# Optimization experiments

Hardware: AMD Instinct MI355X
Metric: run time of the kernel (lower is better)

## Reference

```python
import jax, jax.numpy as jnp
import numpy as np

B, L1, L2, D = 32, 512, 512, 1024


def setup_inputs() -> dict:
    key = jax.random.key(0)
    k1, k2, k3, k4 = jax.random.split(key, 4)
    v1 = jax.random.normal(k1, (B, L1, D), dtype=jnp.float32)
    v2 = jax.random.normal(k2, (B, L2, D), dtype=jnp.float32)
    # row/column is fully masked (which would NaN the softmax).
    v1_mask = jax.random.uniform(k3, (B, L1)) < 0.2
    v2_mask = jax.random.uniform(k4, (B, L2)) < 0.2
    return {"v1": v1, "v2": v2, "v1_mask": v1_mask, "v2_mask": v2_mask}


def reference(v1, v2, v1_mask, v2_mask):
    # similarity: [B, L1, L2]
    sim = jnp.einsum("bid,bjd->bij", v1, v2)
    neg_inf = jnp.float32(-jnp.inf)
    # softmax over v2 positions (dim=2), masking padded v2 columns
    v1_v2_attn = jax.nn.softmax(
        jnp.where(v2_mask[:, None, :], neg_inf, sim), axis=2)
    # softmax over v1 positions (dim=1), masking padded v1 rows
    v2_v1_attn = jax.nn.softmax(
        jnp.where(v1_mask[:, :, None], neg_inf, sim), axis=1)
    attended_v1 = jnp.einsum("bij,bjd->bid", v1_v2_attn, v2)  # [B,L1,D]
    attended_v2 = jnp.einsum("bij,bid->bjd", v2_v1_attn, v1)  # [B,L2,D]
    attended_v1 = jnp.where(v1_mask[:, :, None], 0.0, attended_v1)
    attended_v2 = jnp.where(v2_mask[:, :, None], 0.0, attended_v2)
    return attended_v1, attended_v2
```

## Files before the change

### kernel.cpp

```cpp
#include <hip/hip_runtime.h>
#include <stdint.h>


#define Bn 32
#define Ln 512
#define Dn 1024

typedef __attribute__((ext_vector_type(4))) float f32x4;
typedef __attribute__((ext_vector_type(4))) unsigned short u16x4;
typedef __attribute__((ext_vector_type(8))) unsigned short u16x8;
typedef __attribute__((ext_vector_type(8))) __bf16 bf16x8;

__device__ __forceinline__ unsigned short f2bf(float f) {
  unsigned int u = __float_as_uint(f);
  u += 0x7FFFu + ((u >> 16) & 1u);
  return (unsigned short)(u >> 16);
}

__device__ __forceinline__ void async_cp16(const void* g, void* l) {
  __builtin_amdgcn_global_load_lds(
      (__attribute__((address_space(1))) void*)(g),
      (__attribute__((address_space(3))) void*)(l), 16, 0, 0);
}

__device__ __forceinline__ void split8(f32x4 x0, f32x4 x1,
                                       u16x8* h, u16x8* l) {
  float xs[8] = {x0[0], x0[1], x0[2], x0[3], x1[0], x1[1], x1[2], x1[3]};
  u16x8 hh, ll;
#pragma unroll
  for (int e = 0; e < 8; e++) {
    unsigned int u = __float_as_uint(xs[e]);
    hh[e] = (unsigned short)(u >> 16);
    float hf = __uint_as_float(u & 0xFFFF0000u);
    ll[e] = (unsigned short)(__float_as_uint(xs[e] - hf) >> 16);
  }
  *h = hh;
  *l = ll;
}

__global__ __launch_bounds__(256) void conv_t(
    const float* __restrict__ v1, const float* __restrict__ v2,
    unsigned short* __restrict__ v1t, unsigned short* __restrict__ v2t) {
  __shared__ float tile[64][65];
  const int z = blockIdx.z;
  const float* src = (z < Bn) ? v1 : v2;
  unsigned short* dt = (z < Bn) ? v1t : v2t;
  const int b = z & 31;
  const int d0 = blockIdx.x << 6;
  const int l0 = blockIdx.y << 6;
  const int tid = threadIdx.x;
#pragma unroll
  for (int it = 0; it < 4; it++) {
    int lin = (it << 8) + tid;
    int l = lin >> 4;
    int d4 = (lin & 15) << 2;
    f32x4 x = *(const f32x4*)(src + (size_t)(b * Ln + l0 + l) * Dn + d0 + d4);
    tile[l][d4] = x[0]; tile[l][d4 + 1] = x[1];
    tile[l][d4 + 2] = x[2]; tile[l][d4 + 3] = x[3];
  }
  __syncthreads();
#pragma unroll
  for (int it = 0; it < 4; it++) {
    int lin = (it << 8) + tid;
    int d = lin >> 4;
    int l4 = (lin & 15) << 2;
    u16x4 o;
    o[0] = f2bf(tile[l4][d]);     o[1] = f2bf(tile[l4 + 1][d]);
    o[2] = f2bf(tile[l4 + 2][d]); o[3] = f2bf(tile[l4 + 3][d]);
    *(u16x4*)(dt + (size_t)(b * Dn + d0 + d) * Ln + l0 + l4) = o;
  }
}

__global__ __launch_bounds__(512) void sim_gemm(
    const float* __restrict__ V1, const float* __restrict__ V2,
    float* __restrict__ C, const int* __restrict__ v1m,
    const int* __restrict__ v2m,
    float* __restrict__ pmaxR, float* __restrict__ psumR,
    float* __restrict__ pmaxC, float* __restrict__ psumC) {
  __shared__ __align__(16) unsigned short sAh[8192], sAl[8192];
  __shared__ __align__(16) unsigned short sBh[8192], sBl[8192];
  const int bid = blockIdx.x;
  const int id = ((bid & 7) << 4) + (bid >> 3);
  const int b = id >> 2;
  const int m0 = ((id >> 1) & 1) << 8;
  const int n0 = (id & 1) << 8;
  const int tid = threadIdx.x;
  const int lane = tid & 63;
  const int wave = tid >> 6;
  const int wm = wave >> 2;
  const int wn = wave & 3;
  const int r = lane & 15;
  const int q = lane >> 4;
  const int srow = tid >> 1;
  const int sc0 = (tid & 1) << 1;
  const int ss = (srow >> 1) & 3;
  const size_t bo = (size_t)b * Ln * Dn;
  const float* gA = V1 + bo + (size_t)(m0 + srow) * Dn + (sc0 << 3);
  const float* gB = V2 + bo + (size_t)(n0 + srow) * Dn + (sc0 << 3);
  const int w0 = srow * 32 + ((sc0 ^ ss) << 3);
  const int w1 = srow * 32 + (((sc0 + 1) ^ ss) << 3);

  f32x4 xa[4], xb[4];
#define SIM_LOAD(kk)                                             \
  do {                                                           \
    const float* pa = gA + (kk);                                 \
    const float* pb = gB + (kk);                                 \
    xa[0] = *(const f32x4*)pa;       xa[1] = *(const f32x4*)(pa + 4);  \
    xa[2] = *(const f32x4*)(pa + 8); xa[3] = *(const f32x4*)(pa + 12); \
    xb[0] = *(const f32x4*)pb;       xb[1] = *(const f32x4*)(pb + 4);  \
    xb[2] = *(const f32x4*)(pb + 8); xb[3] = *(const f32x4*)(pb + 12); \
  } while (0)
#define SIM_CVTW()                                               \
  do {                                                           \
    u16x8 h_, l_;                                                \
    split8(xa[0], xa[1], &h_, &l_);                              \
    *(u16x8*)(sAh + w0) = h_; *(u16x8*)(sAl + w0) = l_;          \
    split8(xa[2], xa[3], &h_, &l_);                              \
    *(u16x8*)(sAh + w1) = h_; *(u16x8*)(sAl + w1) = l_;          \
    split8(xb[0], xb[1], &h_, &l_);                              \
    *(u16x8*)(sBh + w0) = h_; *(u16x8*)(sBl + w0) = l_;          \
    split8(xb[2], xb[3], &h_, &l_);                              \
    *(u16x8*)(sBh + w1) = h_; *(u16x8*)(sBl + w1) = l_;          \
  } while (0)

  const f32x4 zero4 = {0.f, 0.f, 0.f, 0.f};
  f32x4 acc[8][4];
#pragma unroll
  for (int i = 0; i < 8; i++)
#pragma unroll
    for (int j = 0; j < 4; j++) acc[i][j] = zero4;

  SIM_LOAD(0);
  SIM_CVTW();
  __syncthreads();

  for (int k0 = 0; k0 < Dn; k0 += 32) {
    const bool more = (k0 + 32 < Dn);
    if (more) SIM_LOAD(k0 + 32);
    bf16x8 bh[4], bl[4];
#pragma unroll
    for (int tn = 0; tn < 4; tn++) {
      int rb = (wn << 6) + (tn << 4) + r;
      int sb = (rb << 5) + ((q ^ ((rb >> 1) & 3)) << 3);
      bh[tn] = *(const bf16x8*)(sBh + sb);
      bl[tn] = *(const bf16x8*)(sBl + sb);
    }
#pragma unroll
    for (int tm = 0; tm < 8; tm++) {
      int ra = (wm << 7) + (tm << 4) + r;
      int sa = (ra << 5) + ((q ^ ((ra >> 1) & 3)) << 3);
      bf16x8 ah = *(const bf16x8*)(sAh + sa);
      bf16x8 al = *(const bf16x8*)(sAl + sa);
#pragma unroll
      for (int tn = 0; tn < 4; tn++) {
        acc[tm][tn] = __builtin_amdgcn_mfma_f32_16x16x32_bf16(
            ah, bh[tn], acc[tm][tn], 0, 0, 0);
        acc[tm][tn] = __builtin_amdgcn_mfma_f32_16x16x32_bf16(
            ah, bl[tn], acc[tm][tn], 0, 0, 0);
        acc[tm][tn] = __builtin_amdgcn_mfma_f32_16x16x32_bf16(
            al, bh[tn], acc[tm][tn], 0, 0, 0);
      }
    }
    __syncthreads();
    if (more) SIM_CVTW();
    __syncthreads();
  }
#undef SIM_LOAD
#undef SIM_CVTW

  float* Cb = C + (size_t)b * Ln * Ln;
#pragma unroll
  for (int tm = 0; tm < 8; tm++) {
    int rowb = m0 + (wm << 7) + (tm << 4) + (q << 2);
#pragma unroll
    for (int reg = 0; reg < 4; reg++) {
      int row = rowb + reg;
#pragma unroll
      for (int tn = 0; tn < 4; tn++) {
        int col = n0 + (wn << 6) + (tn << 4) + r;
        Cb[(size_t)row * Ln + col] = acc[tm][tn][reg];
      }
    }
  }

  const int* mkr = v1m + (b << 9);
  const int* mkc = v2m + (b << 9);
  const float NEGINF = -__builtin_inff();
  unsigned cmb = 0;
#pragma unroll
  for (int tn = 0; tn < 4; tn++)
    cmb |= (mkc[n0 + (wn << 6) + (tn << 4) + r] ? 1u : 0u) << tn;
  unsigned rmb = 0;
#pragma unroll
  for (int t2 = 0; t2 < 32; t2++)
    rmb |= (mkr[m0 + (wm << 7) + ((t2 >> 2) << 4) + (q << 2) + (t2 & 3)]
                ? 1u : 0u) << t2;

  const int nsub = (n0 >> 6) + wn;
#pragma unroll
  for (int tm = 0; tm < 8; tm++) {
#pragma unroll
    for (int reg = 0; reg < 4; reg++) {
      float m = NEGINF;
#pragma unroll
      for (int tn = 0; tn < 4; tn++)
        if (!((cmb >> tn) & 1)) m = fmaxf(m, acc[tm][tn][reg]);
#pragma unroll
      for (int off = 1; off < 16; off <<= 1)
        m = fmaxf(m, __shfl_xor(m, off));
      float s = 0.f;
#pragma unroll
      for (int tn = 0; tn < 4; tn++)
        if (!((cmb >> tn) & 1)) s += __expf(acc[tm][tn][reg] - m);
#pragma unroll
      for (int off = 1; off < 16; off <<= 1) s += __shfl_xor(s, off);
      if (r == 0) {
        int row = m0 + (wm << 7) + (tm << 4) + (q << 2) + reg;
        int idx = (((b << 3) + nsub) << 9) + row;
        pmaxR[idx] = m;
        psumR[idx] = s;
      }
    }
  }

  const int msub = (m0 >> 7) + wm;
#pragma unroll
  for (int tn = 0; tn < 4; tn++) {
    float m = NEGINF;
#pragma unroll
    for (int tm = 0; tm < 8; tm++)
#pragma unroll
      for (int reg = 0; reg < 4; reg++)
        if (!((rmb >> ((tm << 2) + reg)) & 1))
          m = fmaxf(m, acc[tm][tn][reg]);
    m = fmaxf(m, __shfl_xor(m, 16));
    m = fmaxf(m, __shfl_xor(m, 32));
    float s = 0.f;
#pragma unroll
    for (int tm = 0; tm < 8; tm++)
#pragma unroll
      for (int reg = 0; reg < 4; reg++)
        if (!((rmb >> ((tm << 2) + reg)) & 1))
          s += __expf(acc[tm][tn][reg] - m);
    s += __shfl_xor(s, 16);
    s += __shfl_xor(s, 32);
    if (q == 0) {
      int col = n0 + (wn << 6) + (tn << 4) + r;
      int idx = (((b << 2) + msub) << 9) + col;
      pmaxC[idx] = m;
      psumC[idx] = s;
    }
  }
}

__global__ __launch_bounds__(256) void comb(
    const float* __restrict__ pmaxR, const float* __restrict__ psumR,
    const float* __restrict__ pmaxC, const float* __restrict__ psumC,
    float* __restrict__ rowmax, float* __restrict__ rowrs,
    float* __restrict__ colmax, float* __restrict__ colrs) {
  const int id = (blockIdx.x << 8) + threadIdx.x;
  const int side = id >> 14;
  const int x = id & 16383;
  const int bq = x >> 9;
  const int j = x & 511;
  const float NEGINF = -__builtin_inff();
  if (!side) {
    float mm[8], sv[8];
#pragma unroll
    for (int p = 0; p < 8; p++) {
      int idx = (((bq << 3) + p) << 9) + j;
      mm[p] = pmaxR[idx];
      sv[p] = psumR[idx];
    }
    float M = NEGINF;
#pragma unroll
    for (int p = 0; p < 8; p++) M = fmaxf(M, mm[p]);
    float S = 0.f;
#pragma unroll
    for (int p = 0; p < 8; p++)
      S += (mm[p] > NEGINF) ? sv[p] * __expf(mm[p] - M) : 0.f;
    rowmax[x] = M;
    rowrs[x] = 1.f / S;
  } else {
    float mm[4], sv[4];
#pragma unroll
    for (int p = 0; p < 4; p++) {
      int idx = (((bq << 2) + p) << 9) + j;
      mm[p] = pmaxC[idx];
      sv[p] = psumC[idx];
    }
    float M = NEGINF;
#pragma unroll
    for (int p = 0; p < 4; p++) M = fmaxf(M, mm[p]);
    float S = 0.f;
#pragma unroll
    for (int p = 0; p < 4; p++)
      S += (mm[p] > NEGINF) ? sv[p] * __expf(mm[p] - M) : 0.f;
    colmax[x] = M;
    colrs[x] = 1.f / S;
  }
}

__global__ __launch_bounds__(256) void norm_write(
    const float* __restrict__ sim, const int* __restrict__ v1m,
    const int* __restrict__ v2m,
    const float* __restrict__ rowmax, const float* __restrict__ rowrs,
    const float* __restrict__ colmax, const float* __restrict__ colrs,
    unsigned short* __restrict__ A1, unsigned short* __restrict__ A2t) {
  __shared__ unsigned short Tc[64][66];
  __shared__ float rm[64], rr[64], cmx[64], crx[64];
  __shared__ int jmk[64], imk[64];
  const int b = blockIdx.z;
  const int i0 = blockIdx.y << 6;
  const int j0 = blockIdx.x << 6;
  const int tid = threadIdx.x;
  if (tid < 64) {
    cmx[tid] = colmax[(b << 9) + j0 + tid];
    crx[tid] = colrs[(b << 9) + j0 + tid];
  } else if (tid < 128) {
    int t = tid - 64;
    rm[t] = rowmax[(b << 9) + i0 + t];
    rr[t] = rowrs[(b << 9) + i0 + t];
  } else if (tid < 192) {
    jmk[tid - 128] = v2m[(b << 9) + j0 + tid - 128];
  } else {
    imk[tid - 192] = v1m[(b << 9) + i0 + tid - 192];
  }
  __syncthreads();
  const int ri = tid >> 4;
  const int jj = (tid & 15) << 2;
  const float* Sb = sim + (size_t)b * (Ln * Ln);
  unsigned short* A1b = A1 + ((size_t)((b << 9) + i0)) * Ln + j0;
#pragma unroll
  for (int p = 0; p < 4; p++) {
    int il = (p << 4) + ri;
    f32x4 x = *(const f32x4*)(Sb + (size_t)(i0 + il) * Ln + j0 + jj);
    float rmv = rm[il], rrv = rr[il];
    int mrow = imk[il];
    u16x4 o1;
#pragma unroll
    for (int e = 0; e < 4; e++) {
      float e1 = jmk[jj + e] ? 0.f : __expf(x[e] - rmv) * rrv;
      o1[e] = f2bf(e1);
      float e2 = mrow ? 0.f : __expf(x[e] - cmx[jj + e]) * crx[jj + e];
      Tc[jj + e][il] = f2bf(e2);
    }
    *(u16x4*)(A1b + (size_t)il * Ln + jj) = o1;
  }
  __syncthreads();
  unsigned short* o = A2t + ((size_t)((b << 9) + j0)) * Ln + i0;
#pragma unroll
  for (int t = 0; t < 4; t++) {
    int c = (t << 8) + tid;
    int j = c >> 4;
    int ch = c & 15;
    u16x4 v;
    v[0] = Tc[j][(ch << 2)];     v[1] = Tc[j][(ch << 2) + 1];
    v[2] = Tc[j][(ch << 2) + 2]; v[3] = Tc[j][(ch << 2) + 3];
    *(u16x4*)(o + (size_t)j * Ln + (ch << 2)) = v;
  }
}

__global__ __launch_bounds__(256) void gemm_nt2(
    const unsigned short* __restrict__ A1g, const unsigned short* __restrict__ A2tg,
    const unsigned short* __restrict__ v2t, const unsigned short* __restrict__ v1t,
    float* __restrict__ out1, float* __restrict__ out2,
    const int* __restrict__ v1m, const int* __restrict__ v2m) {
  const int Mv = 512, Nv = 1024, Kv = 512;
  __shared__ unsigned short As[2][4096];
  __shared__ unsigned short Bs[2][4096];
  const int bid = blockIdx.x;
  const int id = ((bid & 7) << 8) + (bid >> 3);
  const int z = id >> 5;
  const int m0 = ((id >> 3) & 3) << 7;
  const int n0 = (id & 7) << 7;
  const int b = z & 31;
  const int w2 = z >> 5;
  const unsigned short* A = w2 ? A2tg : A1g;
  const unsigned short* Bm = w2 ? v1t : v2t;
  float* C = w2 ? out2 : out1;
  const int* rowmask = w2 ? v2m : v1m;
  const unsigned short* Ab = A + (size_t)b * Mv * Kv;
  const unsigned short* Bb = Bm + (size_t)b * Nv * Kv;
  float* Cb = C + (size_t)b * Mv * Nv;
  const int tid = threadIdx.x;
  const int lane = tid & 63;
  const int wave = tid >> 6;
  const int wrow = (wave >> 1) << 6;
  const int wcol = (wave & 1) << 6;

  const int srow = tid >> 2;
  const int skof = (tid & 3) << 3;
  const unsigned short* ga0 = Ab + (size_t)(m0 + srow) * Kv + skof;
  const unsigned short* ga1 = Ab + (size_t)(m0 + 64 + srow) * Kv + skof;
  const unsigned short* gb0 = Bb + (size_t)(n0 + srow) * Kv + skof;
  const unsigned short* gb1 = Bb + (size_t)(n0 + 64 + srow) * Kv + skof;
  const int ldsw = wave << 9;

#define PV_STAGE(nb, kk)                            \
  do {                                              \
    async_cp16(ga0 + (kk), &As[nb][ldsw]);          \
    async_cp16(ga1 + (kk), &As[nb][2048 + ldsw]);   \
    async_cp16(gb0 + (kk), &Bs[nb][ldsw]);          \
    async_cp16(gb1 + (kk), &Bs[nb][2048 + ldsw]);   \
  } while (0)

  const int r = lane & 15;
  const int q = lane >> 4;

  const f32x4 zero4 = {0.f, 0.f, 0.f, 0.f};
  f32x4 acc[4][4];
#pragma unroll
  for (int i = 0; i < 4; i++)
#pragma unroll
    for (int j = 0; j < 4; j++) acc[i][j] = zero4;

  PV_STAGE(0, 0);
  __syncthreads();

  int cb = 0;
  for (int k0 = 0; k0 < Kv; k0 += 32, cb ^= 1) {
    if (k0 + 32 < Kv) PV_STAGE(cb ^ 1, k0 + 32);
    bf16x8 af[4], bfr[4];
#pragma unroll
    for (int t = 0; t < 4; t++) {
      af[t] = *(const bf16x8*)(&As[cb][((wrow + (t << 4) + r) << 5) + (q << 3)]);
      bfr[t] = *(const bf16x8*)(&Bs[cb][((wcol + (t << 4) + r) << 5) + (q << 3)]);
    }
#pragma unroll
    for (int tm = 0; tm < 4; tm++)
#pragma unroll
      for (int tn = 0; tn < 4; tn++)
        acc[tm][tn] = __builtin_amdgcn_mfma_f32_16x16x32_bf16(
            af[tm], bfr[tn], acc[tm][tn], 0, 0, 0);
    __syncthreads();
  }
#undef PV_STAGE

  const int* mb = rowmask + b * Mv;
#pragma unroll
  for (int tm = 0; tm < 4; tm++) {
    int rowb = m0 + wrow + (tm << 4) + (q << 2);
#pragma unroll
    for (int reg = 0; reg < 4; reg++) {
      int row = rowb + reg;
      float mz = mb[row] ? 0.f : 1.f;
#pragma unroll
      for (int tn = 0; tn < 4; tn++) {
        int col = n0 + wcol + (tn << 4) + r;
        Cb[(size_t)row * Nv + col] = acc[tm][tn][reg] * mz;
      }
    }
  }
}

extern "C" void kernel_launch(void* const* d_in, const int* in_sizes, int n_in,
                              void* d_out, int out_size, void* d_ws,
                              size_t ws_size, hipStream_t stream) {
  (void)in_sizes; (void)n_in; (void)out_size; (void)ws_size;
  const float* v1 = (const float*)d_in[0];
  const float* v2 = (const float*)d_in[1];
  const int* v1m = (const int*)d_in[2];
  const int* v2m = (const int*)d_in[3];
  float* out1 = (float*)d_out;
  float* out2 = out1 + (size_t)Bn * Ln * Dn;

  char* ws = (char*)d_ws;
  const size_t Mi = 1048576;
  unsigned short* v1t = (unsigned short*)(ws);
  unsigned short* v2t = (unsigned short*)(ws + 32 * Mi);
  float* sim = (float*)(ws + 64 * Mi);
  unsigned short* A1 = (unsigned short*)(ws + 96 * Mi);
  unsigned short* A2t = (unsigned short*)(ws + 112 * Mi);
  float* pmaxR = (float*)(ws + 128 * Mi);
  float* psumR = (float*)(ws + 128 * Mi + 512 * 1024);
  float* pmaxC = (float*)(ws + 129 * Mi);
  float* psumC = (float*)(ws + 129 * Mi + 256 * 1024);
  float* rowmax = (float*)(ws + 129 * Mi + 512 * 1024);
  float* rowrs = (float*)(ws + 129 * Mi + 576 * 1024);
  float* colmax = (float*)(ws + 129 * Mi + 640 * 1024);
  float* colrs = (float*)(ws + 129 * Mi + 704 * 1024);

  dim3 blk(256);
  conv_t<<<dim3(16, 8, 64), blk, 0, stream>>>(v1, v2, v1t, v2t);
  sim_gemm<<<dim3(128), dim3(512), 0, stream>>>(v1, v2, sim, v1m, v2m,
                                                pmaxR, psumR, pmaxC, psumC);
  comb<<<dim3(128), blk, 0, stream>>>(pmaxR, psumR, pmaxC, psumC,
                                      rowmax, rowrs, colmax, colrs);
  norm_write<<<dim3(8, 8, 32), blk, 0, stream>>>(sim, v1m, v2m, rowmax, rowrs,
                                                 colmax, colrs, A1, A2t);
  gemm_nt2<<<dim3(2048), blk, 0, stream>>>(A1, A2t, v2t, v1t,
                                           out1, out2, v1m, v2m);
}
```

Before: 404.9 us.

## Shrink sim GEMM tiles to 128x128, double-buffer LDS, and use native bf16 conversion

The similarity GEMM moves from 128 blocks of 512 threads with 256x256 tiles to 512 blocks of 256 threads with 128x128 tiles. This gives more blocks across the CUs, and the partial softmax stats are adjusted to 8 column-partials per row. The LDS staging is now double-buffered, which removes one barrier per k-step. The hi/lo bf16 split now uses native __bf16 conversion with rounding in place of truncation. The conv_t launch is also reordered after sim_gemm. Smaller tiles mean less operand reuse and more global traffic in exchange for better occupancy and load balance.

```diff
diff --git a/kernel.cpp b/kernel.cpp
--- a/kernel.cpp
+++ b/kernel.cpp
@@ -29,10 +29,12 @@
   u16x8 hh, ll;
 #pragma unroll
   for (int e = 0; e < 8; e++) {
-    unsigned int u = __float_as_uint(xs[e]);
-    hh[e] = (unsigned short)(u >> 16);
-    float hf = __uint_as_float(u & 0xFFFF0000u);
-    ll[e] = (unsigned short)(__float_as_uint(xs[e] - hf) >> 16);
+    union { __bf16 b; unsigned short u; } hc, lc;
+    hc.b = (__bf16)xs[e];
+    float hf = (float)hc.b;
+    lc.b = (__bf16)(xs[e] - hf);
+    hh[e] = hc.u;
+    ll[e] = lc.u;
   }
   *h = hh;
   *l = ll;
@@ -71,86 +73,87 @@
   }
 }
 
-__global__ __launch_bounds__(512) void sim_gemm(
+__global__ __launch_bounds__(256) void sim_gemm(
     const float* __restrict__ V1, const float* __restrict__ V2,
     float* __restrict__ C, const int* __restrict__ v1m,
     const int* __restrict__ v2m,
     float* __restrict__ pmaxR, float* __restrict__ psumR,
     float* __restrict__ pmaxC, float* __restrict__ psumC) {
-  __shared__ __align__(16) unsigned short sAh[8192], sAl[8192];
-  __shared__ __align__(16) unsigned short sBh[8192], sBl[8192];
+  __shared__ __align__(16) unsigned short sAh[2][4096], sAl[2][4096];
+  __shared__ __align__(16) unsigned short sBh[2][4096], sBl[2][4096];
   const int bid = blockIdx.x;
-  const int id = ((bid & 7) << 4) + (bid >> 3);
-  const int b = id >> 2;
-  const int m0 = ((id >> 1) & 1) << 8;
-  const int n0 = (id & 1) << 8;
+  const int id = ((bid & 7) << 6) + (bid >> 3);
+  const int b = id >> 4;
+  const int m0 = ((id >> 2) & 3) << 7;
+  const int n0 = (id & 3) << 7;
   const int tid = threadIdx.x;
   const int lane = tid & 63;
   const int wave = tid >> 6;
-  const int wm = wave >> 2;
-  const int wn = wave & 3;
+  const int wrow = (wave >> 1) << 6;
+  const int wcol = (wave & 1) << 6;
   const int r = lane & 15;
   const int q = lane >> 4;
   const int srow = tid >> 1;
-  const int sc0 = (tid & 1) << 1;
+  const int c0 = (tid & 1) << 1;
   const int ss = (srow >> 1) & 3;
   const size_t bo = (size_t)b * Ln * Dn;
-  const float* gA = V1 + bo + (size_t)(m0 + srow) * Dn + (sc0 << 3);
-  const float* gB = V2 + bo + (size_t)(n0 + srow) * Dn + (sc0 << 3);
-  const int w0 = srow * 32 + ((sc0 ^ ss) << 3);
-  const int w1 = srow * 32 + (((sc0 + 1) ^ ss) << 3);
+  const float* gA = V1 + bo + (size_t)(m0 + srow) * Dn + (c0 << 3);
+  const float* gB = V2 + bo + (size_t)(n0 + srow) * Dn + (c0 << 3);
+  const int w0 = (srow << 5) + (((c0    ) ^ ss) << 3);
+  const int w1 = (srow << 5) + (((c0 + 1) ^ ss) << 3);
 
   f32x4 xa[4], xb[4];
-#define SIM_LOAD(kk)                                             \
-  do {                                                           \
-    const float* pa = gA + (kk);                                 \
-    const float* pb = gB + (kk);                                 \
+#define SIM_LOAD(kk)                                                   \
+  do {                                                                 \
+    const float* pa = gA + (kk);                                       \
+    const float* pb = gB + (kk);                                       \
     xa[0] = *(const f32x4*)pa;       xa[1] = *(const f32x4*)(pa + 4);  \
     xa[2] = *(const f32x4*)(pa + 8); xa[3] = *(const f32x4*)(pa + 12); \
     xb[0] = *(const f32x4*)pb;       xb[1] = *(const f32x4*)(pb + 4);  \
     xb[2] = *(const f32x4*)(pb + 8); xb[3] = *(const f32x4*)(pb + 12); \
   } while (0)
-#define SIM_CVTW()                                               \
-  do {                                                           \
-    u16x8 h_, l_;                                                \
-    split8(xa[0], xa[1], &h_, &l_);                              \
-    *(u16x8*)(sAh + w0) = h_; *(u16x8*)(sAl + w0) = l_;          \
-    split8(xa[2], xa[3], &h_, &l_);                              \
-    *(u16x8*)(sAh + w1) = h_; *(u16x8*)(sAl + w1) = l_;          \
-    split8(xb[0], xb[1], &h_, &l_);                              \
-    *(u16x8*)(sBh + w0) = h_; *(u16x8*)(sBl + w0) = l_;          \
-    split8(xb[2], xb[3], &h_, &l_);                              \
-    *(u16x8*)(sBh + w1) = h_; *(u16x8*)(sBl + w1) = l_;          \
+#define SIM_CVTW(nb)                                                   \
+  do {                                                                 \
+    u16x8 h_, l_;                                                      \
+    split8(xa[0], xa[1], &h_, &l_);                                    \
+    *(u16x8*)(&sAh[nb][w0]) = h_; *(u16x8*)(&sAl[nb][w0]) = l_;        \
+    split8(xa[2], xa[3], &h_, &l_);                                    \
+    *(u16x8*)(&sAh[nb][w1]) = h_; *(u16x8*)(&sAl[nb][w1]) = l_;        \
+    split8(xb[0], xb[1], &h_, &l_);                                    \
+    *(u16x8*)(&sBh[nb][w0]) = h_; *(u16x8*)(&sBl[nb][w0]) = l_;        \
+    split8(xb[2], xb[3], &h_, &l_);                                    \
+    *(u16x8*)(&sBh[nb][w1]) = h_; *(u16x8*)(&sBl[nb][w1]) = l_;        \
   } while (0)
 
   const f32x4 zero4 = {0.f, 0.f, 0.f, 0.f};
-  f32x4 acc[8][4];
-#pragma unroll
-  for (int i = 0; i < 8; i++)
+  f32x4 acc[4][4];
+#pragma unroll
+  for (int i = 0; i < 4; i++)
 #pragma unroll
     for (int j = 0; j < 4; j++) acc[i][j] = zero4;
 
   SIM_LOAD(0);
-  SIM_CVTW();
+  SIM_CVTW(0);
   __syncthreads();
 
-  for (int k0 = 0; k0 < Dn; k0 += 32) {
+  int cb = 0;
+  for (int k0 = 0; k0 < Dn; k0 += 32, cb ^= 1) {
     const bool more = (k0 + 32 < Dn);
     if (more) SIM_LOAD(k0 + 32);
     bf16x8 bh[4], bl[4];
 #pragma unroll
     for (int tn = 0; tn < 4; tn++) {
-      int rb = (wn << 6) + (tn << 4) + r;
+      int rb = wcol + (tn << 4) + r;
       int sb = (rb << 5) + ((q ^ ((rb >> 1) & 3)) << 3);
-      bh[tn] = *(const bf16x8*)(sBh + sb);
-      bl[tn] = *(const bf16x8*)(sBl + sb);
-    }
-#pragma unroll
-    for (int tm = 0; tm < 8; tm++) {
-      int ra = (wm << 7) + (tm << 4) + r;
+      bh[tn] = *(const bf16x8*)(&sBh[cb][sb]);
+      bl[tn] = *(const bf16x8*)(&sBl[cb][sb]);
+    }
+#pragma unroll
+    for (int tm = 0; tm < 4; tm++) {
+      int ra = wrow + (tm << 4) + r;
       int sa = (ra << 5) + ((q ^ ((ra >> 1) & 3)) << 3);
-      bf16x8 ah = *(const bf16x8*)(sAh + sa);
-      bf16x8 al = *(const bf16x8*)(sAl + sa);
+      bf16x8 ah = *(const bf16x8*)(&sAh[cb][sa]);
+      bf16x8 al = *(const bf16x8*)(&sAl[cb][sa]);
 #pragma unroll
       for (int tn = 0; tn < 4; tn++) {
         acc[tm][tn] = __builtin_amdgcn_mfma_f32_16x16x32_bf16(
@@ -161,8 +164,7 @@
             al, bh[tn], acc[tm][tn], 0, 0, 0);
       }
     }
-    __syncthreads();
-    if (more) SIM_CVTW();
+    if (more) SIM_CVTW(cb ^ 1);
     __syncthreads();
   }
 #undef SIM_LOAD
@@ -170,14 +172,14 @@
 
   float* Cb = C + (size_t)b * Ln * Ln;
 #pragma unroll
-  for (int tm = 0; tm < 8; tm++) {
-    int rowb = m0 + (wm << 7) + (tm << 4) + (q << 2);
+  for (int tm = 0; tm < 4; tm++) {
+    int rowb = m0 + wrow + (tm << 4) + (q << 2);
 #pragma unroll
     for (int reg = 0; reg < 4; reg++) {
       int row = rowb + reg;
 #pragma unroll
       for (int tn = 0; tn < 4; tn++) {
-        int col = n0 + (wn << 6) + (tn << 4) + r;
+        int col = n0 + wcol + (tn << 4) + r;
         Cb[(size_t)row * Ln + col] = acc[tm][tn][reg];
       }
     }
@@ -189,16 +191,16 @@
   unsigned cmb = 0;
 #pragma unroll
   for (int tn = 0; tn < 4; tn++)
-    cmb |= (mkc[n0 + (wn << 6) + (tn << 4) + r] ? 1u : 0u) << tn;
+    cmb |= (mkc[n0 + wcol + (tn << 4) + r] ? 1u : 0u) << tn;
   unsigned rmb = 0;
 #pragma unroll
-  for (int t2 = 0; t2 < 32; t2++)
-    rmb |= (mkr[m0 + (wm << 7) + ((t2 >> 2) << 4) + (q << 2) + (t2 & 3)]
-                ? 1u : 0u) << t2;
-
-  const int nsub = (n0 >> 6) + wn;
-#pragma unroll
-  for (int tm = 0; tm < 8; tm++) {
+  for (int t2 = 0; t2 < 16; t2++)
+    rmb |= (mkr[m0 + wrow + ((t2 >> 2) << 4) + (q << 2) + (t2 & 3)] ? 1u : 0u)
+           << t2;
+
+  const int nsub = (n0 + wcol) >> 6;
+#pragma unroll
+  for (int tm = 0; tm < 4; tm++) {
 #pragma unroll
     for (int reg = 0; reg < 4; reg++) {
       float m = NEGINF;
@@ -215,7 +217,7 @@
 #pragma unroll
       for (int off = 1; off < 16; off <<= 1) s += __shfl_xor(s, off);
       if (r == 0) {
-        int row = m0 + (wm << 7) + (tm << 4) + (q << 2) + reg;
+        int row = m0 + wrow + (tm << 4) + (q << 2) + reg;
         int idx = (((b << 3) + nsub) << 9) + row;
         pmaxR[idx] = m;
         psumR[idx] = s;
@@ -223,12 +225,12 @@
     }
   }
 
-  const int msub = (m0 >> 7) + wm;
+  const int msub = (m0 + wrow) >> 6;
 #pragma unroll
   for (int tn = 0; tn < 4; tn++) {
     float m = NEGINF;
 #pragma unroll
-    for (int tm = 0; tm < 8; tm++)
+    for (int tm = 0; tm < 4; tm++)
 #pragma unroll
       for (int reg = 0; reg < 4; reg++)
         if (!((rmb >> ((tm << 2) + reg)) & 1))
@@ -237,7 +239,7 @@
     m = fmaxf(m, __shfl_xor(m, 32));
     float s = 0.f;
 #pragma unroll
-    for (int tm = 0; tm < 8; tm++)
+    for (int tm = 0; tm < 4; tm++)
 #pragma unroll
       for (int reg = 0; reg < 4; reg++)
         if (!((rmb >> ((tm << 2) + reg)) & 1))
@@ -245,8 +247,8 @@
     s += __shfl_xor(s, 16);
     s += __shfl_xor(s, 32);
     if (q == 0) {
-      int col = n0 + (wn << 6) + (tn << 4) + r;
-      int idx = (((b << 2) + msub) << 9) + col;
+      int col = n0 + wcol + (tn << 4) + r;
+      int idx = (((b << 3) + msub) << 9) + col;
       pmaxC[idx] = m;
       psumC[idx] = s;
     }
@@ -261,44 +263,28 @@
   const int id = (blockIdx.x << 8) + threadIdx.x;
   const int side = id >> 14;
   const int x = id & 16383;
+  const float* pm = side ? pmaxC : pmaxR;
+  const float* ps = side ? psumC : psumR;
   const int bq = x >> 9;
   const int j = x & 511;
   const float NEGINF = -__builtin_inff();
-  if (!side) {
-    float mm[8], sv[8];
-#pragma unroll
-    for (int p = 0; p < 8; p++) {
-      int idx = (((bq << 3) + p) << 9) + j;
-      mm[p] = pmaxR[idx];
-      sv[p] = psumR[idx];
-    }
-    float M = NEGINF;
-#pragma unroll
-    for (int p = 0; p < 8; p++) M = fmaxf(M, mm[p]);
-    float S = 0.f;
-#pragma unroll
-    for (int p = 0; p < 8; p++)
-      S += (mm[p] > NEGINF) ? sv[p] * __expf(mm[p] - M) : 0.f;
-    rowmax[x] = M;
-    rowrs[x] = 1.f / S;
-  } else {
-    float mm[4], sv[4];
-#pragma unroll
-    for (int p = 0; p < 4; p++) {
-      int idx = (((bq << 2) + p) << 9) + j;
-      mm[p] = pmaxC[idx];
-      sv[p] = psumC[idx];
-    }
-    float M = NEGINF;
-#pragma unroll
-    for (int p = 0; p < 4; p++) M = fmaxf(M, mm[p]);
-    float S = 0.f;
-#pragma unroll
-    for (int p = 0; p < 4; p++)
-      S += (mm[p] > NEGINF) ? sv[p] * __expf(mm[p] - M) : 0.f;
-    colmax[x] = M;
-    colrs[x] = 1.f / S;
-  }
+  float mm[8], sv[8];
+#pragma unroll
+  for (int p = 0; p < 8; p++) {
+    int idx = (((bq << 3) + p) << 9) + j;
+    mm[p] = pm[idx];
+    sv[p] = ps[idx];
+  }
+  float M = NEGINF;
+#pragma unroll
+  for (int p = 0; p < 8; p++) M = fmaxf(M, mm[p]);
+  float S = 0.f;
+#pragma unroll
+  for (int p = 0; p < 8; p++)
+    S += (mm[p] > NEGINF) ? sv[p] * __expf(mm[p] - M) : 0.f;
+  float rs = 1.f / S;
+  if (side) { colmax[x] = M; colrs[x] = rs; }
+  else      { rowmax[x] = M; rowrs[x] = rs; }
 }
 
 __global__ __launch_bounds__(256) void norm_write(
@@ -475,16 +461,16 @@
   float* pmaxR = (float*)(ws + 128 * Mi);
   float* psumR = (float*)(ws + 128 * Mi + 512 * 1024);
   float* pmaxC = (float*)(ws + 129 * Mi);
-  float* psumC = (float*)(ws + 129 * Mi + 256 * 1024);
-  float* rowmax = (float*)(ws + 129 * Mi + 512 * 1024);
-  float* rowrs = (float*)(ws + 129 * Mi + 576 * 1024);
-  float* colmax = (float*)(ws + 129 * Mi + 640 * 1024);
-  float* colrs = (float*)(ws + 129 * Mi + 704 * 1024);
+  float* psumC = (float*)(ws + 129 * Mi + 512 * 1024);
+  float* rowmax = (float*)(ws + 130 * Mi);
+  float* rowrs = (float*)(ws + 130 * Mi + 64 * 1024);
+  float* colmax = (float*)(ws + 130 * Mi + 128 * 1024);
+  float* colrs = (float*)(ws + 130 * Mi + 192 * 1024);
 
   dim3 blk(256);
+  sim_gemm<<<dim3(512), blk, 0, stream>>>(v1, v2, sim, v1m, v2m,
+                                          pmaxR, psumR, pmaxC, psumC);
   conv_t<<<dim3(16, 8, 64), blk, 0, stream>>>(v1, v2, v1t, v2t);
-  sim_gemm<<<dim3(128), dim3(512), 0, stream>>>(v1, v2, sim, v1m, v2m,
-                                                pmaxR, psumR, pmaxC, psumC);
   comb<<<dim3(128), blk, 0, stream>>>(pmaxR, psumR, pmaxC, psumC,
                                       rowmax, rowrs, colmax, colrs);
   norm_write<<<dim3(8, 8, 32), blk, 0, stream>>>(sim, v1m, v2m, rowmax, rowrs,
```

Measured after the change: 355.1 us. 1.14x faster.
